# Optimization experiments

Hardware: AMD Instinct MI355X
Metric: run time of the kernel (lower is better)

The kernel has to match this reference:

```python
import jax, jax.numpy as jnp
import numpy as np

B, S, H, I, E, K = 2, 2048, 896, 4864, 4, 2


def setup_inputs() -> dict:
    key = jax.random.key(0)
    ks = jax.random.split(key, 5)
    s_h = 1.0 / np.sqrt(H)
    s_i = 1.0 / np.sqrt(I)
    return {
        "x": jax.random.normal(ks[0], (B, S, H), dtype=jnp.float32),
        # torch nn.Linear weights are [out, in]
        "router_w": jax.random.uniform(ks[1], (E, H), dtype=jnp.float32, minval=-s_h, maxval=s_h),
        "gate_w": jax.random.uniform(ks[2], (E, I, H), dtype=jnp.float32, minval=-s_h, maxval=s_h),
        "up_w": jax.random.uniform(ks[3], (E, I, H), dtype=jnp.float32, minval=-s_h, maxval=s_h),
        "down_w": jax.random.uniform(ks[4], (E, H, I), dtype=jnp.float32, minval=-s_i, maxval=s_i),
    }


def reference(x, router_w, gate_w, up_w, down_w):
    # Router: softmax in fp32, top-k, renormalize (matches torch.softmax(dtype=float) + topk)
    logits = jnp.einsum("bsh,eh->bse", x, router_w)
    probs = jax.nn.softmax(logits.astype(jnp.float32), axis=-1)
    top_w, top_i = jax.lax.top_k(probs, K)                      # [B,S,K]
    top_w = top_w / jnp.sum(top_w, axis=-1, keepdims=True)
    # Dense per-expert combine weight: zero for unselected experts
    w_full = jnp.sum(jax.nn.one_hot(top_i, E, dtype=x.dtype) * top_w[..., None].astype(x.dtype), axis=-2)  # [B,S,E]
    # All experts on all tokens (E is small); unselected get weight 0
    gate = jax.nn.silu(jnp.einsum("bsh,eih->bsei", x, gate_w))  # [B,S,E,I]
    up = jnp.einsum("bsh,eih->bsei", x, up_w)
    y = jnp.einsum("bsei,ehi->bseh", gate * up, down_w)          # [B,S,E,H]
    return jnp.einsum("bseh,bse->bsh", y, w_full)
```

## Files before the change

kernel.cpp:

```cpp
#include <hip/hip_runtime.h>
#include <hip/hip_bf16.h>

#define E_ 4
#define H_ 896
#define I_ 4864
#define T_ 4096
#define P_ 8192

typedef unsigned short u16;
typedef __attribute__((ext_vector_type(8))) short short8;
typedef __attribute__((ext_vector_type(4))) float f32x4;

__device__ __forceinline__ void gload16(const void* g, void* l) {
  __builtin_amdgcn_global_load_lds(
      (const __attribute__((address_space(1))) unsigned int*)g,
      (__attribute__((address_space(3))) unsigned int*)l, 16, 0, 0);
}

__device__ __forceinline__ u16 f2bf(float f) {
  unsigned int u = __builtin_bit_cast(unsigned int, f);
  unsigned int r = (u + 0x7FFFu + ((u >> 16) & 1u)) >> 16;
  return (u16)r;
}

__global__ __launch_bounds__(256) void cast_bf16_kernel(const float* __restrict__ in,
                                                        u16* __restrict__ out, long n) {
  long base = ((long)blockIdx.x * 256 + threadIdx.x) * 4;
  if (base + 3 < n) {
    float4 v = *reinterpret_cast<const float4*>(in + base);
    ushort4 o;
    o.x = f2bf(v.x); o.y = f2bf(v.y); o.z = f2bf(v.z); o.w = f2bf(v.w);
    *reinterpret_cast<ushort4*>(out + base) = o;
  } else {
    for (long j = base; j < n; ++j) out[j] = f2bf(in[j]);
  }
}

__global__ __launch_bounds__(64) void router_kernel(const float* __restrict__ x,
                                                    const float* __restrict__ rw,
                                                    int* __restrict__ cnt,
                                                    int* __restrict__ pairs,
                                                    float* __restrict__ wgt) {
  int t = blockIdx.x;
  int lane = threadIdx.x;
  const float* xr = x + (long)t * H_;
  float a0 = 0.f, a1 = 0.f, a2 = 0.f, a3 = 0.f;
  for (int h = lane; h < H_; h += 64) {
    float xv = xr[h];
    a0 += xv * rw[0 * H_ + h];
    a1 += xv * rw[1 * H_ + h];
    a2 += xv * rw[2 * H_ + h];
    a3 += xv * rw[3 * H_ + h];
  }
  for (int off = 32; off > 0; off >>= 1) {
    a0 += __shfl_xor(a0, off, 64);
    a1 += __shfl_xor(a1, off, 64);
    a2 += __shfl_xor(a2, off, 64);
    a3 += __shfl_xor(a3, off, 64);
  }
  if (lane == 0) {
    float l[4] = {a0, a1, a2, a3};
    int i0 = 0;
    for (int e = 1; e < 4; ++e) if (l[e] > l[i0]) i0 = e;
    int i1 = -1;
    for (int e = 0; e < 4; ++e) {
      if (e == i0) continue;
      if (i1 < 0 || l[e] > l[i1]) i1 = e;
    }
    float w0 = 1.0f / (1.0f + __expf(l[i1] - l[i0]));
    int j0 = atomicAdd(&cnt[i0], 1);
    pairs[i0 * T_ + j0] = 2 * t;
    wgt[2 * t] = w0;
    int j1 = atomicAdd(&cnt[i1], 1);
    pairs[i1 * T_ + j1] = 2 * t + 1;
    wgt[2 * t + 1] = 1.0f - w0;
  }
}

__global__ __launch_bounds__(256, 2) void gemm1_kernel(const u16* __restrict__ xb,
                                                       const u16* __restrict__ gw,
                                                       const u16* __restrict__ uw,
                                                       const int* __restrict__ cnt,
                                                       const int* __restrict__ pairs,
                                                       u16* __restrict__ hbuf) {
  int e = blockIdx.z;
  int n = cnt[e];
  int row0 = blockIdx.y * 128;
  if (row0 >= n) return;
  int col0 = blockIdx.x * 128;

  __shared__ alignas(16) u16 As[128 * 32];
  __shared__ alignas(16) u16 Bg[128 * 32];
  __shared__ alignas(16) u16 Bu[128 * 32];
  __shared__ int rows[128];

  int tid = threadIdx.x;
  if (tid < 128) {
    int j = row0 + tid;
    if (j >= n) j = n - 1;
    rows[tid] = pairs[e * T_ + j];
  }
  __syncthreads();

  int rh = tid >> 2;
  int kc = (tid & 3) * 8;
  const u16* ag0 = xb + (long)(rows[rh] >> 1) * H_ + kc;
  const u16* ag1 = xb + (long)(rows[rh + 64] >> 1) * H_ + kc;
  const u16* bg0 = gw + (long)e * I_ * H_ + (long)(col0 + rh) * H_ + kc;
  const u16* bg1 = bg0 + 64L * H_;
  const u16* bu0 = uw + (long)e * I_ * H_ + (long)(col0 + rh) * H_ + kc;
  const u16* bu1 = bu0 + 64L * H_;

  u16* lA0 = As + tid * 8;
  u16* lA1 = As + 2048 + tid * 8;
  u16* lG0 = Bg + tid * 8;
  u16* lG1 = Bg + 2048 + tid * 8;
  u16* lU0 = Bu + tid * 8;
  u16* lU1 = Bu + 2048 + tid * 8;

  f32x4 accg[4][4] = {};
  f32x4 accu[4][4] = {};

  int lane = tid & 63;
  int wave = tid >> 6;
  int wm = (wave >> 1) * 64;
  int wn = (wave & 1) * 64;
  int lm = lane & 15;
  int lk = (lane >> 4) * 8;

  for (int kt = 0; kt < H_; kt += 32) {
    __syncthreads();
    gload16(ag0 + kt, lA0);
    gload16(ag1 + kt, lA1);
    gload16(bg0 + kt, lG0);
    gload16(bg1 + kt, lG1);
    gload16(bu0 + kt, lU0);
    gload16(bu1 + kt, lU1);
    __syncthreads();

    short8 af[4];
#pragma unroll
    for (int bi = 0; bi < 4; ++bi)
      af[bi] = *reinterpret_cast<const short8*>(&As[(wm + bi * 16 + lm) * 32 + lk]);
#pragma unroll
    for (int bj = 0; bj < 4; ++bj) {
      short8 bgf = *reinterpret_cast<const short8*>(&Bg[(wn + bj * 16 + lm) * 32 + lk]);
      short8 buf = *reinterpret_cast<const short8*>(&Bu[(wn + bj * 16 + lm) * 32 + lk]);
#pragma unroll
      for (int bi = 0; bi < 4; ++bi) {
        accg[bi][bj] = __builtin_amdgcn_mfma_f32_16x16x32_bf16(af[bi], bgf, accg[bi][bj], 0, 0, 0);
        accu[bi][bj] = __builtin_amdgcn_mfma_f32_16x16x32_bf16(af[bi], buf, accu[bi][bj], 0, 0, 0);
      }
    }
  }

  int rq = (lane >> 4) * 4;
#pragma unroll
  for (int bi = 0; bi < 4; ++bi) {
#pragma unroll
    for (int r = 0; r < 4; ++r) {
      int rloc = wm + bi * 16 + rq + r;
      if (row0 + rloc < n) {
        long p = rows[rloc];
        u16* hr = hbuf + p * (long)I_ + col0 + wn + lm;
#pragma unroll
        for (int bj = 0; bj < 4; ++bj) {
          float g = accg[bi][bj][r];
          float u = accu[bi][bj][r];
          float s = g / (1.0f + __expf(-g));
          hr[bj * 16] = f2bf(s * u);
        }
      }
    }
  }
}

__global__ __launch_bounds__(256, 2) void gemm2_kernel(const u16* __restrict__ hbuf,
                                                       const u16* __restrict__ dw,
                                                       const int* __restrict__ cnt,
                                                       const int* __restrict__ pairs,
                                                       const float* __restrict__ wgt,
                                                       float* __restrict__ out) {
  int e = blockIdx.z;
  int n = cnt[e];
  int row0 = blockIdx.y * 128;
  if (row0 >= n) return;
  int col0 = blockIdx.x * 128;

  __shared__ alignas(16) u16 As[128 * 32];
  __shared__ alignas(16) u16 Bs[128 * 32];
  __shared__ int rows[128];

  int tid = threadIdx.x;
  if (tid < 128) {
    int j = row0 + tid;
    if (j >= n) j = n - 1;
    rows[tid] = pairs[e * T_ + j];
  }
  __syncthreads();

  int rh = tid >> 2;
  int kc = (tid & 3) * 8;
  const u16* ag0 = hbuf + (long)rows[rh] * I_ + kc;
  const u16* ag1 = hbuf + (long)rows[rh + 64] * I_ + kc;
  const u16* bg0 = dw + (long)e * H_ * I_ + (long)(col0 + rh) * I_ + kc;
  const u16* bg1 = bg0 + 64L * I_;

  u16* lA0 = As + tid * 8;
  u16* lA1 = As + 2048 + tid * 8;
  u16* lB0 = Bs + tid * 8;
  u16* lB1 = Bs + 2048 + tid * 8;

  f32x4 acc[4][4] = {};

  int lane = tid & 63;
  int wave = tid >> 6;
  int wm = (wave >> 1) * 64;
  int wn = (wave & 1) * 64;
  int lm = lane & 15;
  int lk = (lane >> 4) * 8;

  for (int kt = 0; kt < I_; kt += 32) {
    __syncthreads();
    gload16(ag0 + kt, lA0);
    gload16(ag1 + kt, lA1);
    gload16(bg0 + kt, lB0);
    gload16(bg1 + kt, lB1);
    __syncthreads();

    short8 af[4];
#pragma unroll
    for (int bi = 0; bi < 4; ++bi)
      af[bi] = *reinterpret_cast<const short8*>(&As[(wm + bi * 16 + lm) * 32 + lk]);
#pragma unroll
    for (int bj = 0; bj < 4; ++bj) {
      short8 bf = *reinterpret_cast<const short8*>(&Bs[(wn + bj * 16 + lm) * 32 + lk]);
#pragma unroll
      for (int bi = 0; bi < 4; ++bi)
        acc[bi][bj] = __builtin_amdgcn_mfma_f32_16x16x32_bf16(af[bi], bf, acc[bi][bj], 0, 0, 0);
    }
  }

  int rq = (lane >> 4) * 4;
#pragma unroll
  for (int bi = 0; bi < 4; ++bi) {
#pragma unroll
    for (int r = 0; r < 4; ++r) {
      int rloc = wm + bi * 16 + rq + r;
      if (row0 + rloc < n) {
        int p = rows[rloc];
        int t = p >> 1;
        float w = wgt[p];
        float* orow = out + (long)t * H_ + col0 + wn + lm;
#pragma unroll
        for (int bj = 0; bj < 4; ++bj)
          atomicAdd(&orow[bj * 16], w * acc[bi][bj][r]);
      }
    }
  }
}

extern "C" void kernel_launch(void* const* d_in, const int* in_sizes, int n_in,
                              void* d_out, int out_size, void* d_ws, size_t ws_size,
                              hipStream_t stream) {
  const float* x        = (const float*)d_in[0];
  const float* router_w = (const float*)d_in[1];
  const float* gate_w   = (const float*)d_in[2];
  const float* up_w     = (const float*)d_in[3];
  const float* down_w   = (const float*)d_in[4];
  float* out = (float*)d_out;

  const long WN = (long)E_ * I_ * H_;

  char* ws = (char*)d_ws;
  size_t off = 0;
  auto alloc = [&](size_t bytes) {
    void* p = ws + off;
    off = (off + bytes + 255) & ~(size_t)255;
    return p;
  };
  u16* gw_b  = (u16*)alloc(WN * 2);
  u16* uw_b  = (u16*)alloc(WN * 2);
  u16* dw_b  = (u16*)alloc(WN * 2);
  u16* xb    = (u16*)alloc((long)T_ * H_ * 2);
  u16* hbuf  = (u16*)alloc((long)P_ * I_ * 2);
  int* cnt   = (int*)alloc(256);
  int* pairs = (int*)alloc((long)E_ * T_ * 4);
  float* wgt = (float*)alloc((long)P_ * 4);

  hipMemsetAsync(cnt, 0, 256, stream);
  hipMemsetAsync(d_out, 0, (size_t)out_size * sizeof(float), stream);

  cast_bf16_kernel<<<WN / 1024, 256, 0, stream>>>(gate_w, gw_b, WN);
  cast_bf16_kernel<<<WN / 1024, 256, 0, stream>>>(up_w, uw_b, WN);
  cast_bf16_kernel<<<WN / 1024, 256, 0, stream>>>(down_w, dw_b, WN);
  cast_bf16_kernel<<<((long)T_ * H_) / 1024, 256, 0, stream>>>(x, xb, (long)T_ * H_);

  router_kernel<<<T_, 64, 0, stream>>>(x, router_w, cnt, pairs, wgt);

  dim3 g1(I_ / 128, T_ / 128, E_);
  gemm1_kernel<<<g1, 256, 0, stream>>>(xb, gw_b, uw_b, cnt, pairs, hbuf);

  dim3 g2(H_ / 128, T_ / 128, E_);
  gemm2_kernel<<<g2, 256, 0, stream>>>(hbuf, dw_b, cnt, pairs, wgt, out);
}
```

Measured before the change: 743.8 us.

## Widen K tile to 64 with XOR-swizzled LDS and split-K gemm2

Both GEMMs now stage a 64-wide K slice per iteration instead of 32, halving the number of barrier pairs, and place the data in LDS with an XOR swizzle so the fragment reads avoid bank conflicts. gemm2 also splits its K dimension in two across blockIdx.z, doubling the grid to fill more CUs, and raises its occupancy hint to 3. The split relies on the existing atomicAdd epilogue to merge partial sums, which doubles the atomic traffic to the output.

Result: faster. 659.1 us (-11.4%).

```diff
diff --git a/kernel.cpp b/kernel.cpp
--- a/kernel.cpp
+++ b/kernel.cpp
@@ -6,6 +6,7 @@
 #define I_ 4864
 #define T_ 4096
 #define P_ 8192
+#define KS2 2432
 
 typedef unsigned short u16;
 typedef __attribute__((ext_vector_type(8))) short short8;
@@ -77,6 +78,7 @@
   }
 }
 
+
 __global__ __launch_bounds__(256, 2) void gemm1_kernel(const u16* __restrict__ xb,
                                                        const u16* __restrict__ gw,
                                                        const u16* __restrict__ uw,
@@ -89,9 +91,9 @@
   if (row0 >= n) return;
   int col0 = blockIdx.x * 128;
 
-  __shared__ alignas(16) u16 As[128 * 32];
-  __shared__ alignas(16) u16 Bg[128 * 32];
-  __shared__ alignas(16) u16 Bu[128 * 32];
+  __shared__ alignas(16) u16 As[128 * 64];
+  __shared__ alignas(16) u16 Bg[128 * 64];
+  __shared__ alignas(16) u16 Bu[128 * 64];
   __shared__ int rows[128];
 
   int tid = threadIdx.x;
@@ -102,21 +104,23 @@
   }
   __syncthreads();
 
-  int rh = tid >> 2;
-  int kc = (tid & 3) * 8;
-  const u16* ag0 = xb + (long)(rows[rh] >> 1) * H_ + kc;
-  const u16* ag1 = xb + (long)(rows[rh + 64] >> 1) * H_ + kc;
-  const u16* bg0 = gw + (long)e * I_ * H_ + (long)(col0 + rh) * H_ + kc;
-  const u16* bg1 = bg0 + 64L * H_;
-  const u16* bu0 = uw + (long)e * I_ * H_ + (long)(col0 + rh) * H_ + kc;
-  const u16* bu1 = bu0 + 64L * H_;
-
-  u16* lA0 = As + tid * 8;
-  u16* lA1 = As + 2048 + tid * 8;
-  u16* lG0 = Bg + tid * 8;
-  u16* lG1 = Bg + 2048 + tid * 8;
-  u16* lU0 = Bu + tid * 8;
-  u16* lU1 = Bu + 2048 + tid * 8;
+  int rr = tid >> 3;
+  int cc = tid & 7;
+  long eoff = (long)e * I_ * H_;
+
+  const u16* aP[4]; const u16* gP[4]; const u16* uP[4];
+  u16* lA[4]; u16* lG[4]; u16* lU[4];
+#pragma unroll
+  for (int q = 0; q < 4; ++q) {
+    int gr = rr + 32 * q;
+    int g8 = (cc ^ (gr & 7)) * 8;
+    aP[q] = xb + (long)(rows[gr] >> 1) * H_ + g8;
+    gP[q] = gw + eoff + (long)(col0 + gr) * H_ + g8;
+    uP[q] = uw + eoff + (long)(col0 + gr) * H_ + g8;
+    lA[q] = As + q * 2048 + tid * 8;
+    lG[q] = Bg + q * 2048 + tid * 8;
+    lU[q] = Bu + q * 2048 + tid * 8;
+  }
 
   f32x4 accg[4][4] = {};
   f32x4 accu[4][4] = {};
@@ -126,30 +130,35 @@
   int wm = (wave >> 1) * 64;
   int wn = (wave & 1) * 64;
   int lm = lane & 15;
-  int lk = (lane >> 4) * 8;
-
-  for (int kt = 0; kt < H_; kt += 32) {
+  int qv = lane >> 4;
+  int px = qv ^ (lm & 7);
+
+  for (int kt = 0; kt < H_; kt += 64) {
     __syncthreads();
-    gload16(ag0 + kt, lA0);
-    gload16(ag1 + kt, lA1);
-    gload16(bg0 + kt, lG0);
-    gload16(bg1 + kt, lG1);
-    gload16(bu0 + kt, lU0);
-    gload16(bu1 + kt, lU1);
+#pragma unroll
+    for (int q = 0; q < 4; ++q) {
+      gload16(aP[q] + kt, lA[q]);
+      gload16(gP[q] + kt, lG[q]);
+      gload16(uP[q] + kt, lU[q]);
+    }
     __syncthreads();
 
-    short8 af[4];
-#pragma unroll
-    for (int bi = 0; bi < 4; ++bi)
-      af[bi] = *reinterpret_cast<const short8*>(&As[(wm + bi * 16 + lm) * 32 + lk]);
-#pragma unroll
-    for (int bj = 0; bj < 4; ++bj) {
-      short8 bgf = *reinterpret_cast<const short8*>(&Bg[(wn + bj * 16 + lm) * 32 + lk]);
-      short8 buf = *reinterpret_cast<const short8*>(&Bu[(wn + bj * 16 + lm) * 32 + lk]);
-#pragma unroll
-      for (int bi = 0; bi < 4; ++bi) {
-        accg[bi][bj] = __builtin_amdgcn_mfma_f32_16x16x32_bf16(af[bi], bgf, accg[bi][bj], 0, 0, 0);
-        accu[bi][bj] = __builtin_amdgcn_mfma_f32_16x16x32_bf16(af[bi], buf, accu[bi][bj], 0, 0, 0);
+#pragma unroll
+    for (int kh = 0; kh < 2; ++kh) {
+      int po = (px ^ (kh << 2)) * 8;
+      short8 af[4];
+#pragma unroll
+      for (int bi = 0; bi < 4; ++bi)
+        af[bi] = *reinterpret_cast<const short8*>(&As[(wm + bi * 16 + lm) * 64 + po]);
+#pragma unroll
+      for (int bj = 0; bj < 4; ++bj) {
+        short8 bgf = *reinterpret_cast<const short8*>(&Bg[(wn + bj * 16 + lm) * 64 + po]);
+        short8 buf = *reinterpret_cast<const short8*>(&Bu[(wn + bj * 16 + lm) * 64 + po]);
+#pragma unroll
+        for (int bi = 0; bi < 4; ++bi) {
+          accg[bi][bj] = __builtin_amdgcn_mfma_f32_16x16x32_bf16(af[bi], bgf, accg[bi][bj], 0, 0, 0);
+          accu[bi][bj] = __builtin_amdgcn_mfma_f32_16x16x32_bf16(af[bi], buf, accu[bi][bj], 0, 0, 0);
+        }
       }
     }
   }
@@ -175,20 +184,22 @@
   }
 }
 
-__global__ __launch_bounds__(256, 2) void gemm2_kernel(const u16* __restrict__ hbuf,
+__global__ __launch_bounds__(256, 3) void gemm2_kernel(const u16* __restrict__ hbuf,
                                                        const u16* __restrict__ dw,
                                                        const int* __restrict__ cnt,
                                                        const int* __restrict__ pairs,
                                                        const float* __restrict__ wgt,
                                                        float* __restrict__ out) {
-  int e = blockIdx.z;
+  int z = blockIdx.z;
+  int e = z >> 1;
+  int k0 = (z & 1) * KS2;
   int n = cnt[e];
   int row0 = blockIdx.y * 128;
   if (row0 >= n) return;
   int col0 = blockIdx.x * 128;
 
-  __shared__ alignas(16) u16 As[128 * 32];
-  __shared__ alignas(16) u16 Bs[128 * 32];
+  __shared__ alignas(16) u16 As[128 * 64];
+  __shared__ alignas(16) u16 Bs[128 * 64];
   __shared__ int rows[128];
 
   int tid = threadIdx.x;
@@ -199,17 +210,20 @@
   }
   __syncthreads();
 
-  int rh = tid >> 2;
-  int kc = (tid & 3) * 8;
-  const u16* ag0 = hbuf + (long)rows[rh] * I_ + kc;
-  const u16* ag1 = hbuf + (long)rows[rh + 64] * I_ + kc;
-  const u16* bg0 = dw + (long)e * H_ * I_ + (long)(col0 + rh) * I_ + kc;
-  const u16* bg1 = bg0 + 64L * I_;
-
-  u16* lA0 = As + tid * 8;
-  u16* lA1 = As + 2048 + tid * 8;
-  u16* lB0 = Bs + tid * 8;
-  u16* lB1 = Bs + 2048 + tid * 8;
+  int rr = tid >> 3;
+  int cc = tid & 7;
+
+  const u16* aP[4]; const u16* bP[4];
+  u16* lA[4]; u16* lB[4];
+#pragma unroll
+  for (int q = 0; q < 4; ++q) {
+    int gr = rr + 32 * q;
+    int g8 = (cc ^ (gr & 7)) * 8;
+    aP[q] = hbuf + (long)rows[gr] * I_ + k0 + g8;
+    bP[q] = dw + (long)e * H_ * I_ + (long)(col0 + gr) * I_ + k0 + g8;
+    lA[q] = As + q * 2048 + tid * 8;
+    lB[q] = Bs + q * 2048 + tid * 8;
+  }
 
   f32x4 acc[4][4] = {};
 
@@ -218,26 +232,32 @@
   int wm = (wave >> 1) * 64;
   int wn = (wave & 1) * 64;
   int lm = lane & 15;
-  int lk = (lane >> 4) * 8;
-
-  for (int kt = 0; kt < I_; kt += 32) {
+  int qv = lane >> 4;
+  int px = qv ^ (lm & 7);
+
+  for (int kt = 0; kt < KS2; kt += 64) {
     __syncthreads();
-    gload16(ag0 + kt, lA0);
-    gload16(ag1 + kt, lA1);
-    gload16(bg0 + kt, lB0);
-    gload16(bg1 + kt, lB1);
+#pragma unroll
+    for (int q = 0; q < 4; ++q) {
+      gload16(aP[q] + kt, lA[q]);
+      gload16(bP[q] + kt, lB[q]);
+    }
     __syncthreads();
 
-    short8 af[4];
-#pragma unroll
-    for (int bi = 0; bi < 4; ++bi)
-      af[bi] = *reinterpret_cast<const short8*>(&As[(wm + bi * 16 + lm) * 32 + lk]);
-#pragma unroll
-    for (int bj = 0; bj < 4; ++bj) {
-      short8 bf = *reinterpret_cast<const short8*>(&Bs[(wn + bj * 16 + lm) * 32 + lk]);
+#pragma unroll
+    for (int kh = 0; kh < 2; ++kh) {
+      int po = (px ^ (kh << 2)) * 8;
+      short8 af[4];
 #pragma unroll
       for (int bi = 0; bi < 4; ++bi)
-        acc[bi][bj] = __builtin_amdgcn_mfma_f32_16x16x32_bf16(af[bi], bf, acc[bi][bj], 0, 0, 0);
+        af[bi] = *reinterpret_cast<const short8*>(&As[(wm + bi * 16 + lm) * 64 + po]);
+#pragma unroll
+      for (int bj = 0; bj < 4; ++bj) {
+        short8 bf = *reinterpret_cast<const short8*>(&Bs[(wn + bj * 16 + lm) * 64 + po]);
+#pragma unroll
+        for (int bi = 0; bi < 4; ++bi)
+          acc[bi][bj] = __builtin_amdgcn_mfma_f32_16x16x32_bf16(af[bi], bf, acc[bi][bj], 0, 0, 0);
+      }
     }
   }
 
@@ -301,6 +321,6 @@
   dim3 g1(I_ / 128, T_ / 128, E_);
   gemm1_kernel<<<g1, 256, 0, stream>>>(xb, gw_b, uw_b, cnt, pairs, hbuf);
 
-  dim3 g2(H_ / 128, T_ / 128, E_);
+  dim3 g2(H_ / 128, T_ / 128, E_ * 2);
   gemm2_kernel<<<g2, 256, 0, stream>>>(hbuf, dw_b, cnt, pairs, wgt, out);
 }
```
